# Kernel optimization log

Measured on AMD Instinct MI355X. Metric: run time of the kernel, lower is better.

## Reference

```python
import jax, jax.numpy as jnp
import numpy as np


def conv2d_nchw(x, w, b, padding):
    # x: [B,Cin,H,W], w: [Cout,Cin,kh,kw]
    y = jax.lax.conv_general_dilated(
        x, w, window_strides=(1, 1), padding=padding,
        dimension_numbers=("NCHW", "OIHW", "NCHW"))
    return y + b[None, :, None, None]


def setup_inputs() -> dict:
    key = jax.random.key(0)
    ks = jax.random.split(key, 8)
    B, C, H, W = 8, 512, 50, 76
    A = 9  # 3 scales x 3 ratios
    base_feat = jax.random.normal(ks[0], (B, C, H, W), dtype=jnp.float32)
    im_info = jnp.tile(jnp.array([800.0, 1216.0, 1.0], jnp.float32), (B, 1))
    gt_boxes = jax.random.uniform(ks[1], (B, 20, 5), dtype=jnp.float32) * 100.0
    num_boxes = jax.random.randint(ks[2], (B,), 1, 20, dtype=jnp.int32)
    # learned parameters (Kaiming-ish small init)
    conv_w = jax.random.normal(ks[3], (512, C, 3, 3), dtype=jnp.float32) * 0.01
    conv_b = jnp.zeros((512,), jnp.float32)
    cls_w = jax.random.normal(ks[4], (2 * A, 512, 1, 1), dtype=jnp.float32) * 0.01
    cls_b = jnp.zeros((2 * A,), jnp.float32)
    bbox_w = jax.random.normal(ks[5], (4 * A, 512, 1, 1), dtype=jnp.float32) * 0.01
    bbox_b = jnp.zeros((4 * A,), jnp.float32)
    return dict(base_feat=base_feat, im_info=im_info, gt_boxes=gt_boxes,
                num_boxes=num_boxes, conv_w=conv_w, conv_b=conv_b,
                cls_w=cls_w, cls_b=cls_b, bbox_w=bbox_w, bbox_b=bbox_b)


def reference(base_feat, im_info, gt_boxes, num_boxes,
              conv_w, conv_b, cls_w, cls_b, bbox_w, bbox_b):
    # RPN_Conv 3x3 + ReLU
    rpn_conv = jax.nn.relu(conv2d_nchw(base_feat, conv_w, conv_b, "SAME"))
    # 1x1 cls head -> [B, 2A, H, W]
    rpn_cls_score = conv2d_nchw(rpn_conv, cls_w, cls_b, "VALID")
    B, C2, H, W = rpn_cls_score.shape
    # _RPN.reshape(x, 2): view as [B, 2, A*H, W], softmax over the 2-way dim
    score_rs = rpn_cls_score.reshape(B, 2, (C2 // 2) * H, W)
    prob_rs = jax.nn.softmax(score_rs, axis=1)
    rpn_cls_prob = prob_rs.reshape(B, C2, H, W)
    # 1x1 bbox head -> [B, 4A, H, W]
    rpn_bbox_pred = conv2d_nchw(rpn_conv, bbox_w, bbox_b, "VALID")
    return rpn_cls_prob, rpn_bbox_pred
```

## Files before the change

### kernel.cpp

```cpp
#include <hip/hip_runtime.h>
#include <hip/hip_bf16.h>


typedef __bf16 bf16_t;
typedef __attribute__((ext_vector_type(8))) __bf16 bf16x8;
typedef __attribute__((ext_vector_type(4))) __bf16 bf16x4;
typedef __attribute__((ext_vector_type(4))) float f32x4;

#define HW 3800
#define NPOS (8 * HW)
#define XP_IMG (52 * 78 * 512)

__device__ __forceinline__ void gload_lds16(const bf16_t* g, char* l) {
  __builtin_amdgcn_global_load_lds(
      (const __attribute__((address_space(1))) unsigned int*)g,
      (__attribute__((address_space(3))) unsigned int*)l, 16, 0, 0);
}

__global__ __launch_bounds__(256) void pad_nhwc(const float* __restrict__ x,
                                                bf16_t* __restrict__ Xp) {
  const int t = threadIdx.x;
  const int blk = blockIdx.x;
  if (blk < 1600) {
    __shared__ __align__(16) bf16_t tile[76][136];
    const int cb = blk & 3;
    int r = blk >> 2;
    const int h = r % 50, b = r / 50;
#pragma unroll
    for (int it = 0; it < 10; ++it) {
      int idx = it * 256 + t;
      if (idx < 2432) {
        int c = idx / 19, w4 = idx - c * 19;
        const float4 v = *(const float4*)(x +
            (((size_t)(b * 512 + cb * 128 + c)) * 50 + h) * 76 + w4 * 4);
        tile[w4 * 4 + 0][c] = (bf16_t)v.x;
        tile[w4 * 4 + 1][c] = (bf16_t)v.y;
        tile[w4 * 4 + 2][c] = (bf16_t)v.z;
        tile[w4 * 4 + 3][c] = (bf16_t)v.w;
      }
    }
    __syncthreads();
#pragma unroll
    for (int it = 0; it < 5; ++it) {
      int idx = it * 256 + t;
      if (idx < 1216) {
        int w = idx >> 4, c8 = idx & 15;
        bf16x8 v = *(const bf16x8*)&tile[w][c8 * 8];
        *(bf16x8*)(Xp + ((size_t)(b * 52 + h + 1) * 78 + (w + 1)) * 512 +
                   cb * 128 + c8 * 8) = v;
      }
    }
  } else {
    const int blk2 = blk - 1600;
    const int b = blk2 >> 1, half = blk2 & 1;
    bf16x8 z;
#pragma unroll
    for (int j = 0; j < 8; ++j) z[j] = (bf16_t)0.f;
#pragma unroll
    for (int it = 0; it < 32; ++it) {
      int idx = it * 256 + t;
      int q = half * 128 + (idx >> 6);
      int c8 = idx & 63;
      int h, w;
      if (q < 78)       { h = 0;           w = q; }
      else if (q < 156) { h = 51;          w = q - 78; }
      else if (q < 206) { h = q - 156 + 1; w = 0; }
      else              { h = q - 206 + 1; w = 77; }
      *(bf16x8*)(Xp + ((size_t)(b * 52 + h) * 78 + w) * 512 + c8 * 8) = z;
    }
  }
}

__global__ __launch_bounds__(256) void wtrans(const float* __restrict__ cw,
                                              bf16_t* __restrict__ Wt) {
  __shared__ bf16_t lw[4608];
  const int t = threadIdx.x;
  const int co = blockIdx.x;
  const float* src = cw + (size_t)co * 4608;
#pragma unroll
  for (int it = 0; it < 18; ++it) {
    int idx = it * 256 + t;
    lw[idx] = (bf16_t)src[idx];
  }
  __syncthreads();
#pragma unroll
  for (int s = 0; s < 9; ++s) {
    int ci = t * 2;
    bf16_t v0 = lw[ci * 9 + s], v1 = lw[(ci + 1) * 9 + s];
    bf16_t* dst = Wt + ((size_t)s * 512 + co) * 512 + ci;
    dst[0] = v0; dst[1] = v1;
  }
}

__global__ __launch_bounds__(256) void whb_build(const float* __restrict__ clsw,
                                                 const float* __restrict__ boxw,
                                                 bf16_t* __restrict__ Whb) {
  int t = blockIdx.x * 256 + threadIdx.x;
  int ci = t & 511; int row = t >> 9;
  float v = 0.f;
  if (row < 18) {
    int a = row >> 1, logit = row & 1;
    v = clsw[(logit * 9 + a) * 512 + ci];
  } else if (row < 54) {
    v = boxw[(row - 18) * 512 + ci];
  }
  Whb[(size_t)row * 512 + ci] = (bf16_t)v;
}

__global__ __launch_bounds__(512) void conv3x3(const bf16_t* __restrict__ Xp,
                                               const bf16_t* __restrict__ Wt,
                                               const float* __restrict__ convb,
                                               bf16_t* __restrict__ rc2) {
  __shared__ __align__(16) char smem[131072];
  const int tid = threadIdx.x;
  const int lane = tid & 63;
  const int wv = tid >> 6;
  const int wm = wv >> 2;
  const int wn = wv & 3;
  const int lm = lane & 15, lg = lane >> 4;

  const int raw = blockIdx.x;
  const int wg = (raw & 7) * 30 + (raw >> 3);
  const int b = wg / 30;
  const int rem = wg - b * 30;
  const int co_base = (rem & 1) * 256;
  const int pos_base = (rem >> 1) * 256;

  int aSrc[4], hB[4], wB[4], cB[4];
#pragma unroll
  for (int i = 0; i < 4; ++i) {
    int d = i * 512 + tid;
    int r = d >> 3, p = d & 7, c = p ^ (r & 7);
    aSrc[i] = (co_base + r) * 512 + c * 8;
    int m = pos_base + r; if (m > HW - 1) m = HW - 1;
    hB[i] = m / 76; wB[i] = m - (m / 76) * 76; cB[i] = c * 8;
  }
  const bf16_t* XpB = Xp + (size_t)b * XP_IMG;

  int aOff[8], bOff[4], koffs[2];
#pragma unroll
  for (int m = 0; m < 8; ++m) aOff[m] = (wm * 128 + m * 16 + lm) * 128;
#pragma unroll
  for (int n = 0; n < 4; ++n) bOff[n] = 32768 + (wn * 64 + n * 16 + lm) * 128;
#pragma unroll
  for (int ks = 0; ks < 2; ++ks) koffs[ks] = ((ks * 4 + lg) ^ (lm & 7)) << 4;

  f32x4 acc[8][4];
#pragma unroll
  for (int i = 0; i < 8; ++i)
#pragma unroll
    for (int j = 0; j < 4; ++j) acc[i][j] = (f32x4){0.f, 0.f, 0.f, 0.f};

#pragma unroll
  for (int i = 0; i < 4; ++i)
    gload_lds16(Wt + aSrc[i], smem + (i * 512 + tid) * 16);
#pragma unroll
  for (int i = 0; i < 4; ++i)
    gload_lds16(XpB + (hB[i] * 78 + wB[i]) * 512 + cB[i],
                smem + 32768 + (i * 512 + tid) * 16);
  asm volatile("s_waitcnt vmcnt(0)" ::: "memory");
  __builtin_amdgcn_s_barrier();
  __builtin_amdgcn_sched_barrier(0);

  for (int kt = 0; kt < 72; ++kt) {
    const int cur = kt & 1;
    const char* Ab = smem + cur * 65536;
    char* Anxt = smem + (cur ^ 1) * 65536;
    const int tn = kt + 1;
    const int sn = tn >> 3, cbn = tn & 7;

    bf16x8 pa[4], pb[4];

    if (tn < 72) {
      const bf16_t* As = Wt + (size_t)sn * 262144 + cbn * 64;
#pragma unroll
      for (int i = 0; i < 4; ++i)
        gload_lds16(As + aSrc[i], Anxt + (i * 512 + tid) * 16);
    }
#pragma unroll
    for (int n = 0; n < 4; ++n) pb[n] = *(const bf16x8*)(Ab + bOff[n] + koffs[0]);
#pragma unroll
    for (int f = 0; f < 4; ++f) pa[f] = *(const bf16x8*)(Ab + aOff[f] + koffs[0]);
    __builtin_amdgcn_s_setprio(1);
#pragma unroll
    for (int f = 0; f < 4; ++f)
#pragma unroll
      for (int n = 0; n < 4; ++n)
        acc[f][n] = __builtin_amdgcn_mfma_f32_16x16x32_bf16(pa[f], pb[n], acc[f][n], 0, 0, 0);
    __builtin_amdgcn_s_setprio(0);
    __builtin_amdgcn_s_barrier();

    if (tn < 72) {
      const int kh = sn / 3, kw = sn - kh * 3;
#pragma unroll
      for (int i = 0; i < 4; ++i) {
        int off = ((hB[i] + kh) * 78 + (wB[i] + kw)) * 512 + cB[i] + cbn * 64;
        gload_lds16(XpB + off, Anxt + 32768 + (i * 512 + tid) * 16);
      }
    }
#pragma unroll
    for (int f = 0; f < 4; ++f) pa[f] = *(const bf16x8*)(Ab + aOff[4 + f] + koffs[0]);
    __builtin_amdgcn_s_setprio(1);
#pragma unroll
    for (int f = 0; f < 4; ++f)
#pragma unroll
      for (int n = 0; n < 4; ++n)
        acc[4 + f][n] = __builtin_amdgcn_mfma_f32_16x16x32_bf16(pa[f], pb[n], acc[4 + f][n], 0, 0, 0);
    __builtin_amdgcn_s_setprio(0);
    __builtin_amdgcn_s_barrier();

#pragma unroll
    for (int n = 0; n < 4; ++n) pb[n] = *(const bf16x8*)(Ab + bOff[n] + koffs[1]);
#pragma unroll
    for (int f = 0; f < 4; ++f) pa[f] = *(const bf16x8*)(Ab + aOff[f] + koffs[1]);
    __builtin_amdgcn_s_setprio(1);
#pragma unroll
    for (int f = 0; f < 4; ++f)
#pragma unroll
      for (int n = 0; n < 4; ++n)
        acc[f][n] = __builtin_amdgcn_mfma_f32_16x16x32_bf16(pa[f], pb[n], acc[f][n], 0, 0, 0);
    __builtin_amdgcn_s_setprio(0);
    __builtin_amdgcn_s_barrier();

#pragma unroll
    for (int f = 0; f < 4; ++f) pa[f] = *(const bf16x8*)(Ab + aOff[4 + f] + koffs[1]);
    __builtin_amdgcn_s_setprio(1);
#pragma unroll
    for (int f = 0; f < 4; ++f)
#pragma unroll
      for (int n = 0; n < 4; ++n)
        acc[4 + f][n] = __builtin_amdgcn_mfma_f32_16x16x32_bf16(pa[f], pb[n], acc[4 + f][n], 0, 0, 0);
    __builtin_amdgcn_s_setprio(0);

    asm volatile("s_waitcnt vmcnt(0)" ::: "memory");
    __builtin_amdgcn_s_barrier();
    __builtin_amdgcn_sched_barrier(0);
  }

  const size_t outRow = (size_t)b * HW;
#pragma unroll
  for (int m = 0; m < 8; ++m) {
    const int co = co_base + wm * 128 + m * 16 + lg * 4;
    const float4 bias = *(const float4*)(convb + co);
#pragma unroll
    for (int n = 0; n < 4; ++n) {
      const int pos = pos_base + wn * 64 + n * 16 + lm;
      if (pos < HW) {
        bf16x4 v;
        float z0 = acc[m][n][0] + bias.x; v[0] = (bf16_t)(z0 > 0.f ? z0 : 0.f);
        float z1 = acc[m][n][1] + bias.y; v[1] = (bf16_t)(z1 > 0.f ? z1 : 0.f);
        float z2 = acc[m][n][2] + bias.z; v[2] = (bf16_t)(z2 > 0.f ? z2 : 0.f);
        float z3 = acc[m][n][3] + bias.w; v[3] = (bf16_t)(z3 > 0.f ? z3 : 0.f);
        *(bf16x4*)(rc2 + (outRow + pos) * 512 + co) = v;
      }
    }
  }
}

__global__ __launch_bounds__(256) void heads_mfma(const bf16_t* __restrict__ rc2,
                                                  const bf16_t* __restrict__ Whb,
                                                  const float* __restrict__ clsb,
                                                  const float* __restrict__ boxb,
                                                  float* __restrict__ out) {
  __shared__ __align__(16) char smem[24576];
  const int t = threadIdx.x, lane = t & 63, wv = t >> 6;
  const int lm = lane & 15, lg = lane >> 4, lx = lane & 7;
  const int pos_base = blockIdx.x * 128;

  int aSrc[2], bSrc[4];
#pragma unroll
  for (int i = 0; i < 2; ++i) {
    int d = i * 256 + t;
    int r = d >> 3, p = d & 7, c = p ^ (r & 7);
    aSrc[i] = r * 512 + c * 8;
  }
#pragma unroll
  for (int i = 0; i < 4; ++i) {
    int d = i * 256 + t;
    int r = d >> 3, p = d & 7, c = p ^ (r & 7);
    int pg = pos_base + r; if (pg > NPOS - 1) pg = NPOS - 1;
    bSrc[i] = pg * 512 + c * 8;
  }

  f32x4 acc[4][2];
#pragma unroll
  for (int i = 0; i < 4; ++i)
#pragma unroll
    for (int j = 0; j < 2; ++j) acc[i][j] = (f32x4){0.f, 0.f, 0.f, 0.f};

  for (int cb = 0; cb < 8; ++cb) {
    __syncthreads();
#pragma unroll
    for (int i = 0; i < 2; ++i) {
      int d = i * 256 + t;
      gload_lds16(Whb + aSrc[i] + cb * 64, &smem[d * 16]);
    }
#pragma unroll
    for (int i = 0; i < 4; ++i) {
      int d = i * 256 + t;
      gload_lds16(rc2 + (size_t)bSrc[i] + cb * 64, &smem[8192 + d * 16]);
    }
    __syncthreads();
#pragma unroll
    for (int ks = 0; ks < 2; ++ks) {
      const int koff = ((ks * 4 + lg) ^ lx) << 4;
      bf16x8 af[4], bfr[2];
#pragma unroll
      for (int f = 0; f < 4; ++f)
        af[f] = *(const bf16x8*)&smem[(f * 16 + lm) * 128 + koff];
#pragma unroll
      for (int f = 0; f < 2; ++f)
        bfr[f] = *(const bf16x8*)&smem[8192 + (wv * 32 + f * 16 + lm) * 128 + koff];
#pragma unroll
      for (int fa = 0; fa < 4; ++fa)
#pragma unroll
        for (int fb = 0; fb < 2; ++fb)
          acc[fa][fb] = __builtin_amdgcn_mfma_f32_16x16x32_bf16(
              af[fa], bfr[fb], acc[fa][fb], 0, 0, 0);
    }
  }

  float* boxOut = out + (size_t)8 * 18 * HW;
#pragma unroll
  for (int fb = 0; fb < 2; ++fb) {
    const int pg = pos_base + wv * 32 + fb * 16 + lm;
    if (pg < NPOS) {
      const int b = pg / HW;
      const int m = pg - b * HW;
#pragma unroll
      for (int fa = 0; fa < 4; ++fa) {
        const int base = fa * 16 + lg * 4;
#pragma unroll
        for (int pr = 0; pr < 2; ++pr) {
          const int row0 = base + pr * 2;
          const float v0 = acc[fa][fb][pr * 2];
          const float v1 = acc[fa][fb][pr * 2 + 1];
          if (row0 < 18) {
            const int a = row0 >> 1;
            const float s0 = v0 + clsb[a];
            const float s1 = v1 + clsb[9 + a];
            const float mx = fmaxf(s0, s1);
            const float e0 = expf(s0 - mx), e1 = expf(s1 - mx);
            const float inv = 1.0f / (e0 + e1);
            out[((size_t)(b * 18 + a)) * HW + m] = e0 * inv;
            out[((size_t)(b * 18 + 9 + a)) * HW + m] = e1 * inv;
          } else if (row0 < 54) {
            const int c0 = row0 - 18;
            boxOut[((size_t)(b * 36 + c0)) * HW + m] = v0 + boxb[c0];
            boxOut[((size_t)(b * 36 + c0 + 1)) * HW + m] = v1 + boxb[c0 + 1];
          }
        }
      }
    }
  }
}

extern "C" void kernel_launch(void* const* d_in, const int* in_sizes, int n_in,
                              void* d_out, int out_size, void* d_ws, size_t ws_size,
                              hipStream_t stream) {
  (void)in_sizes; (void)n_in; (void)out_size; (void)ws_size;
  const float* base_feat = (const float*)d_in[0];
  const float* conv_w = (const float*)d_in[4];
  const float* conv_b = (const float*)d_in[5];
  const float* cls_w  = (const float*)d_in[6];
  const float* cls_b  = (const float*)d_in[7];
  const float* bbox_w = (const float*)d_in[8];
  const float* bbox_b = (const float*)d_in[9];

  char* ws = (char*)d_ws;
  bf16_t* Xp  = (bf16_t*)(ws);
  bf16_t* Wt  = (bf16_t*)(ws + 33226752);
  bf16_t* rc2 = (bf16_t*)(ws + 37945344);
  bf16_t* Whb = (bf16_t*)(ws + 69074944);

  hipLaunchKernelGGL(pad_nhwc,   dim3(1616), dim3(256), 0, stream, base_feat, Xp);
  hipLaunchKernelGGL(wtrans,     dim3(512),  dim3(256), 0, stream, conv_w, Wt);
  hipLaunchKernelGGL(whb_build,  dim3(128),  dim3(256), 0, stream, cls_w, bbox_w, Whb);
  hipLaunchKernelGGL(conv3x3,    dim3(240),  dim3(512), 0, stream, Xp, Wt, conv_b, rc2);
  hipLaunchKernelGGL(heads_mfma, dim3(238),  dim3(256), 0, stream, rc2, Whb, cls_b, bbox_b,
                     (float*)d_out);
}
```

Baseline: 162.1 us.

## Switch conv3x3 mainloop to triple-buffered K=32 stages with prefetch depth two

```diff
diff --git a/kernel.cpp b/kernel.cpp
--- a/kernel.cpp
+++ b/kernel.cpp
@@ -111,7 +111,7 @@
                                                const bf16_t* __restrict__ Wt,
                                                const float* __restrict__ convb,
                                                bf16_t* __restrict__ rc2) {
-  __shared__ __align__(16) char smem[131072];
+  __shared__ __align__(16) char smem[98304];
   const int tid = threadIdx.x;
   const int lane = tid & 63;
   const int wv = tid >> 6;
@@ -126,24 +126,23 @@
   const int co_base = (rem & 1) * 256;
   const int pos_base = (rem >> 1) * 256;
 
-  int aSrc[4], hB[4], wB[4], cB[4];
-#pragma unroll
-  for (int i = 0; i < 4; ++i) {
+  int aSrcRow[2], hB2[2], wB2[2], cB2[2];
+#pragma unroll
+  for (int i = 0; i < 2; ++i) {
     int d = i * 512 + tid;
-    int r = d >> 3, p = d & 7, c = p ^ (r & 7);
-    aSrc[i] = (co_base + r) * 512 + c * 8;
+    int r = d >> 2, p = d & 3, c = p ^ ((r >> 1) & 3);
+    aSrcRow[i] = (co_base + r) * 512 + c * 8;
     int m = pos_base + r; if (m > HW - 1) m = HW - 1;
-    hB[i] = m / 76; wB[i] = m - (m / 76) * 76; cB[i] = c * 8;
+    hB2[i] = m / 76; wB2[i] = m - (m / 76) * 76; cB2[i] = c * 8;
   }
   const bf16_t* XpB = Xp + (size_t)b * XP_IMG;
 
-  int aOff[8], bOff[4], koffs[2];
-#pragma unroll
-  for (int m = 0; m < 8; ++m) aOff[m] = (wm * 128 + m * 16 + lm) * 128;
-#pragma unroll
-  for (int n = 0; n < 4; ++n) bOff[n] = 32768 + (wn * 64 + n * 16 + lm) * 128;
-#pragma unroll
-  for (int ks = 0; ks < 2; ++ks) koffs[ks] = ((ks * 4 + lg) ^ (lm & 7)) << 4;
+  const int koff = (lg ^ ((lm >> 1) & 3)) << 4;
+  int aOffF[8], bOffF[4];
+#pragma unroll
+  for (int m = 0; m < 8; ++m) aOffF[m] = (wm * 128 + m * 16 + lm) * 64 + koff;
+#pragma unroll
+  for (int n = 0; n < 4; ++n) bOffF[n] = 16384 + (wn * 64 + n * 16 + lm) * 64 + koff;
 
   f32x4 acc[8][4];
 #pragma unroll
@@ -151,91 +150,71 @@
 #pragma unroll
     for (int j = 0; j < 4; ++j) acc[i][j] = (f32x4){0.f, 0.f, 0.f, 0.f};
 
-#pragma unroll
-  for (int i = 0; i < 4; ++i)
-    gload_lds16(Wt + aSrc[i], smem + (i * 512 + tid) * 16);
-#pragma unroll
-  for (int i = 0; i < 4; ++i)
-    gload_lds16(XpB + (hB[i] * 78 + wB[i]) * 512 + cB[i],
-                smem + 32768 + (i * 512 + tid) * 16);
-  asm volatile("s_waitcnt vmcnt(0)" ::: "memory");
+#define ISSUE_STAGE(KT, BASE) {                                                   \
+    const int s_ = (KT) >> 4, cb_ = (KT) & 15;                                    \
+    const int kh_ = s_ / 3, kw_ = s_ - kh_ * 3;                                   \
+    const bf16_t* As_ = Wt + (size_t)s_ * 262144 + cb_ * 32;                      \
+    _Pragma("unroll")                                                             \
+    for (int i = 0; i < 2; ++i)                                                   \
+      gload_lds16(As_ + aSrcRow[i], smem + (BASE) + (i * 512 + tid) * 16);        \
+    _Pragma("unroll")                                                             \
+    for (int i = 0; i < 2; ++i)                                                   \
+      gload_lds16(XpB + ((hB2[i] + kh_) * 78 + (wB2[i] + kw_)) * 512 + cB2[i] +   \
+                      cb_ * 32,                                                   \
+                  smem + (BASE) + 16384 + (i * 512 + tid) * 16);                  \
+  }
+
+#define TILE(KT, CURB, NXTB, DO_ISSUE, LAST) {                                    \
+    if (DO_ISSUE) ISSUE_STAGE((KT) + 2, NXTB);                                    \
+    const char* Ab_ = smem + (CURB);                                              \
+    bf16x8 pb_[4], pa_[4];                                                        \
+    _Pragma("unroll")                                                             \
+    for (int n = 0; n < 4; ++n) pb_[n] = *(const bf16x8*)(Ab_ + bOffF[n]);        \
+    _Pragma("unroll")                                                             \
+    for (int f = 0; f < 4; ++f) pa_[f] = *(const bf16x8*)(Ab_ + aOffF[f]);        \
+    __builtin_amdgcn_s_setprio(1);                                                \
+    _Pragma("unroll")                                                             \
+    for (int f = 0; f < 4; ++f)                                                   \
+      _Pragma("unroll")                                                           \
+      for (int n = 0; n < 4; ++n)                                                 \
+        acc[f][n] = __builtin_amdgcn_mfma_f32_16x16x32_bf16(pa_[f], pb_[n],       \
+                                                            acc[f][n], 0, 0, 0); \
+    __builtin_amdgcn_s_setprio(0);                                                \
+    _Pragma("unroll")                                                             \
+    for (int f = 0; f < 4; ++f) pa_[f] = *(const bf16x8*)(Ab_ + aOffF[4 + f]);    \
+    __builtin_amdgcn_s_setprio(1);                                                \
+    _Pragma("unroll")                                                             \
+    for (int f = 0; f < 4; ++f)                                                   \
+      _Pragma("unroll")                                                           \
+      for (int n = 0; n < 4; ++n)                                                 \
+        acc[4 + f][n] = __builtin_amdgcn_mfma_f32_16x16x32_bf16(pa_[f], pb_[n],   \
+                                                          acc[4 + f][n], 0, 0, 0);\
+    __builtin_amdgcn_s_setprio(0);                                                \
+    if (!(LAST)) {                                                                \
+      if (DO_ISSUE) { asm volatile("s_waitcnt vmcnt(4)" ::: "memory"); }          \
+      else          { asm volatile("s_waitcnt vmcnt(0)" ::: "memory"); }          \
+      __builtin_amdgcn_s_barrier();                                               \
+      __builtin_amdgcn_sched_barrier(0);                                          \
+    }                                                                             \
+  }
+
+  ISSUE_STAGE(0, 0);
+  ISSUE_STAGE(1, 32768);
+  asm volatile("s_waitcnt vmcnt(4)" ::: "memory");
   __builtin_amdgcn_s_barrier();
   __builtin_amdgcn_sched_barrier(0);
 
-  for (int kt = 0; kt < 72; ++kt) {
-    const int cur = kt & 1;
-    const char* Ab = smem + cur * 65536;
-    char* Anxt = smem + (cur ^ 1) * 65536;
-    const int tn = kt + 1;
-    const int sn = tn >> 3, cbn = tn & 7;
-
-    bf16x8 pa[4], pb[4];
-
-    if (tn < 72) {
-      const bf16_t* As = Wt + (size_t)sn * 262144 + cbn * 64;
-#pragma unroll
-      for (int i = 0; i < 4; ++i)
-        gload_lds16(As + aSrc[i], Anxt + (i * 512 + tid) * 16);
-    }
-#pragma unroll
-    for (int n = 0; n < 4; ++n) pb[n] = *(const bf16x8*)(Ab + bOff[n] + koffs[0]);
-#pragma unroll
-    for (int f = 0; f < 4; ++f) pa[f] = *(const bf16x8*)(Ab + aOff[f] + koffs[0]);
-    __builtin_amdgcn_s_setprio(1);
-#pragma unroll
-    for (int f = 0; f < 4; ++f)
-#pragma unroll
-      for (int n = 0; n < 4; ++n)
-        acc[f][n] = __builtin_amdgcn_mfma_f32_16x16x32_bf16(pa[f], pb[n], acc[f][n], 0, 0, 0);
-    __builtin_amdgcn_s_setprio(0);
-    __builtin_amdgcn_s_barrier();
-
-    if (tn < 72) {
-      const int kh = sn / 3, kw = sn - kh * 3;
-#pragma unroll
-      for (int i = 0; i < 4; ++i) {
-        int off = ((hB[i] + kh) * 78 + (wB[i] + kw)) * 512 + cB[i] + cbn * 64;
-        gload_lds16(XpB + off, Anxt + 32768 + (i * 512 + tid) * 16);
-      }
-    }
-#pragma unroll
-    for (int f = 0; f < 4; ++f) pa[f] = *(const bf16x8*)(Ab + aOff[4 + f] + koffs[0]);
-    __builtin_amdgcn_s_setprio(1);
-#pragma unroll
-    for (int f = 0; f < 4; ++f)
-#pragma unroll
-      for (int n = 0; n < 4; ++n)
-        acc[4 + f][n] = __builtin_amdgcn_mfma_f32_16x16x32_bf16(pa[f], pb[n], acc[4 + f][n], 0, 0, 0);
-    __builtin_amdgcn_s_setprio(0);
-    __builtin_amdgcn_s_barrier();
-
-#pragma unroll
-    for (int n = 0; n < 4; ++n) pb[n] = *(const bf16x8*)(Ab + bOff[n] + koffs[1]);
-#pragma unroll
-    for (int f = 0; f < 4; ++f) pa[f] = *(const bf16x8*)(Ab + aOff[f] + koffs[1]);
-    __builtin_amdgcn_s_setprio(1);
-#pragma unroll
-    for (int f = 0; f < 4; ++f)
-#pragma unroll
-      for (int n = 0; n < 4; ++n)
-        acc[f][n] = __builtin_amdgcn_mfma_f32_16x16x32_bf16(pa[f], pb[n], acc[f][n], 0, 0, 0);
-    __builtin_amdgcn_s_setprio(0);
-    __builtin_amdgcn_s_barrier();
-
-#pragma unroll
-    for (int f = 0; f < 4; ++f) pa[f] = *(const bf16x8*)(Ab + aOff[4 + f] + koffs[1]);
-    __builtin_amdgcn_s_setprio(1);
-#pragma unroll
-    for (int f = 0; f < 4; ++f)
-#pragma unroll
-      for (int n = 0; n < 4; ++n)
-        acc[4 + f][n] = __builtin_amdgcn_mfma_f32_16x16x32_bf16(pa[f], pb[n], acc[4 + f][n], 0, 0, 0);
-    __builtin_amdgcn_s_setprio(0);
-
-    asm volatile("s_waitcnt vmcnt(0)" ::: "memory");
-    __builtin_amdgcn_s_barrier();
-    __builtin_amdgcn_sched_barrier(0);
-  }
+  for (int kt = 0; kt < 141; kt += 3) {
+    TILE(kt + 0, 0,     65536, true, false);
+    TILE(kt + 1, 32768, 0,     true, false);
+    TILE(kt + 2, 65536, 32768, true, false);
+  }
+  TILE(141, 0,     65536, true,  false);
+  TILE(142, 32768, 0,     false, false);
+  TILE(143, 65536, 32768, false, true);
+
+#undef TILE
+#undef ISSUE_STAGE
 
   const size_t outRow = (size_t)b * HW;
 #pragma unroll
```

New measurement: 164.2 us. About the same (+1.3%).

## Prefetch two K-tiles ahead in conv3x3 with in-place staged LDS reloads

Applied to the files above, without the earlier changes.

```diff
diff --git a/kernel.cpp b/kernel.cpp
--- a/kernel.cpp
+++ b/kernel.cpp
@@ -107,10 +107,10 @@
   Whb[(size_t)row * 512 + ci] = (bf16_t)v;
 }
 
-__global__ __launch_bounds__(512) void conv3x3(const bf16_t* __restrict__ Xp,
-                                               const bf16_t* __restrict__ Wt,
-                                               const float* __restrict__ convb,
-                                               bf16_t* __restrict__ rc2) {
+__global__ __launch_bounds__(512, 2) void conv3x3(const bf16_t* __restrict__ Xp,
+                                                  const bf16_t* __restrict__ Wt,
+                                                  const float* __restrict__ convb,
+                                                  bf16_t* __restrict__ rc2) {
   __shared__ __align__(16) char smem[131072];
   const int tid = threadIdx.x;
   const int lane = tid & 63;
@@ -125,25 +125,38 @@
   const int rem = wg - b * 30;
   const int co_base = (rem & 1) * 256;
   const int pos_base = (rem >> 1) * 256;
-
-  int aSrc[4], hB[4], wB[4], cB[4];
+  const bf16_t* XpB = Xp + (size_t)b * XP_IMG;
+
+  int aSrc[4];
 #pragma unroll
   for (int i = 0; i < 4; ++i) {
     int d = i * 512 + tid;
-    int r = d >> 3, p = d & 7, c = p ^ (r & 7);
+    int r = d >> 3, c = (d & 7) ^ (r & 7);
     aSrc[i] = (co_base + r) * 512 + c * 8;
-    int m = pos_base + r; if (m > HW - 1) m = HW - 1;
-    hB[i] = m / 76; wB[i] = m - (m / 76) * 76; cB[i] = c * 8;
-  }
-  const bf16_t* XpB = Xp + (size_t)b * XP_IMG;
-
-  int aOff[8], bOff[4], koffs[2];
+  }
+  int bSpa[2][2], bCc[2][2], bDst[2][2];
+#pragma unroll
+  for (int f = 0; f < 2; ++f)
+#pragma unroll
+    for (int i = 0; i < 2; ++i) {
+      int d = i * 512 + tid;
+      int rl = d >> 3;
+      int rp = ((rl >> 5) << 6) + f * 32 + (rl & 31);
+      int c = (d & 7) ^ (rp & 7);
+      int m = pos_base + rp; if (m > HW - 1) m = HW - 1;
+      int h = m / 76, w = m - (m / 76) * 76;
+      bSpa[f][i] = h * 78 + w;
+      bCc[f][i] = c * 8;
+      bDst[f][i] = rp * 128 + (d & 7) * 16;
+    }
+
+  const int koff0 = (lg ^ (lm & 7)) << 4;
+  const int koff1 = ((4 + lg) ^ (lm & 7)) << 4;
+  int aOff[8], bOff[4];
 #pragma unroll
   for (int m = 0; m < 8; ++m) aOff[m] = (wm * 128 + m * 16 + lm) * 128;
 #pragma unroll
   for (int n = 0; n < 4; ++n) bOff[n] = 32768 + (wn * 64 + n * 16 + lm) * 128;
-#pragma unroll
-  for (int ks = 0; ks < 2; ++ks) koffs[ks] = ((ks * 4 + lg) ^ (lm & 7)) << 4;
 
   f32x4 acc[8][4];
 #pragma unroll
@@ -151,91 +164,116 @@
 #pragma unroll
     for (int j = 0; j < 4; ++j) acc[i][j] = (f32x4){0.f, 0.f, 0.f, 0.f};
 
-#pragma unroll
-  for (int i = 0; i < 4; ++i)
-    gload_lds16(Wt + aSrc[i], smem + (i * 512 + tid) * 16);
-#pragma unroll
-  for (int i = 0; i < 4; ++i)
-    gload_lds16(XpB + (hB[i] * 78 + wB[i]) * 512 + cB[i],
-                smem + 32768 + (i * 512 + tid) * 16);
-  asm volatile("s_waitcnt vmcnt(0)" ::: "memory");
+#define STAGE_A(KT, BASE) {                                                     \
+    const int s_ = (KT) >> 3, cb_ = (KT) & 7;                                   \
+    const bf16_t* As_ = Wt + (size_t)s_ * 262144 + cb_ * 64;                    \
+    _Pragma("unroll")                                                           \
+    for (int i_ = 0; i_ < 4; ++i_)                                              \
+      gload_lds16(As_ + aSrc[i_], (BASE) + (i_ * 512 + tid) * 16);              \
+  }
+#define STAGE_B(KT, BASE, F) {                                                  \
+    const int s_ = (KT) >> 3, cb_ = (KT) & 7;                                   \
+    const int sp_ = (s_ / 3) * 78 + (s_ - (s_ / 3) * 3);                        \
+    _Pragma("unroll")                                                           \
+    for (int i_ = 0; i_ < 2; ++i_)                                              \
+      gload_lds16(XpB + (size_t)(bSpa[F][i_] + sp_) * 512 + bCc[F][i_] +        \
+                      cb_ * 64,                                                 \
+                  (BASE) + 32768 + bDst[F][i_]);                                \
+  }
+
+  STAGE_A(0, smem);        STAGE_B(0, smem, 0);        STAGE_B(0, smem, 1);
+  STAGE_A(1, smem + 65536); STAGE_B(1, smem + 65536, 0); STAGE_B(1, smem + 65536, 1);
+  asm volatile("s_waitcnt vmcnt(8)" ::: "memory");
   __builtin_amdgcn_s_barrier();
   __builtin_amdgcn_sched_barrier(0);
 
-  for (int kt = 0; kt < 72; ++kt) {
-    const int cur = kt & 1;
-    const char* Ab = smem + cur * 65536;
-    char* Anxt = smem + (cur ^ 1) * 65536;
-    const int tn = kt + 1;
-    const int sn = tn >> 3, cbn = tn & 7;
-
-    bf16x8 pa[4], pb[4];
-
-    if (tn < 72) {
-      const bf16_t* As = Wt + (size_t)sn * 262144 + cbn * 64;
-#pragma unroll
-      for (int i = 0; i < 4; ++i)
-        gload_lds16(As + aSrc[i], Anxt + (i * 512 + tid) * 16);
-    }
-#pragma unroll
-    for (int n = 0; n < 4; ++n) pb[n] = *(const bf16x8*)(Ab + bOff[n] + koffs[0]);
-#pragma unroll
-    for (int f = 0; f < 4; ++f) pa[f] = *(const bf16x8*)(Ab + aOff[f] + koffs[0]);
+  bf16x8 ar[4][2], br[4][2];
+  for (int t = 0; t < 72; ++t) {
+    char* base = smem + (t & 1) * 65536;
+    const int tn = t + 2;
+    const bool st = (tn < 72);
+
+#pragma unroll
+    for (int n = 0; n < 2; ++n) {
+      br[n][0] = *(const bf16x8*)(base + bOff[n] + koff0);
+      br[n][1] = *(const bf16x8*)(base + bOff[n] + koff1);
+    }
+#pragma unroll
+    for (int m = 0; m < 4; ++m) {
+      ar[m][0] = *(const bf16x8*)(base + aOff[m] + koff0);
+      ar[m][1] = *(const bf16x8*)(base + aOff[m] + koff1);
+    }
     __builtin_amdgcn_s_setprio(1);
 #pragma unroll
-    for (int f = 0; f < 4; ++f)
-#pragma unroll
-      for (int n = 0; n < 4; ++n)
-        acc[f][n] = __builtin_amdgcn_mfma_f32_16x16x32_bf16(pa[f], pb[n], acc[f][n], 0, 0, 0);
+    for (int m = 0; m < 4; ++m)
+#pragma unroll
+      for (int n = 0; n < 2; ++n)
+#pragma unroll
+        for (int ks = 0; ks < 2; ++ks)
+          acc[m][n] = __builtin_amdgcn_mfma_f32_16x16x32_bf16(
+              ar[m][ks], br[n][ks], acc[m][n], 0, 0, 0);
     __builtin_amdgcn_s_setprio(0);
     __builtin_amdgcn_s_barrier();
-
-    if (tn < 72) {
-      const int kh = sn / 3, kw = sn - kh * 3;
-#pragma unroll
-      for (int i = 0; i < 4; ++i) {
-        int off = ((hB[i] + kh) * 78 + (wB[i] + kw)) * 512 + cB[i] + cbn * 64;
-        gload_lds16(XpB + off, Anxt + 32768 + (i * 512 + tid) * 16);
-      }
-    }
-#pragma unroll
-    for (int f = 0; f < 4; ++f) pa[f] = *(const bf16x8*)(Ab + aOff[4 + f] + koffs[0]);
+    __builtin_amdgcn_sched_barrier(0);
+
+    if (st) STAGE_B(tn, base, 0);
+#pragma unroll
+    for (int n = 2; n < 4; ++n) {
+      br[n][0] = *(const bf16x8*)(base + bOff[n] + koff0);
+      br[n][1] = *(const bf16x8*)(base + bOff[n] + koff1);
+    }
     __builtin_amdgcn_s_setprio(1);
 #pragma unroll
-    for (int f = 0; f < 4; ++f)
-#pragma unroll
-      for (int n = 0; n < 4; ++n)
-        acc[4 + f][n] = __builtin_amdgcn_mfma_f32_16x16x32_bf16(pa[f], pb[n], acc[4 + f][n], 0, 0, 0);
+    for (int m = 0; m < 4; ++m)
+#pragma unroll
+      for (int n = 2; n < 4; ++n)
+#pragma unroll
+        for (int ks = 0; ks < 2; ++ks)
+          acc[m][n] = __builtin_amdgcn_mfma_f32_16x16x32_bf16(
+              ar[m][ks], br[n][ks], acc[m][n], 0, 0, 0);
     __builtin_amdgcn_s_setprio(0);
     __builtin_amdgcn_s_barrier();
-
-#pragma unroll
-    for (int n = 0; n < 4; ++n) pb[n] = *(const bf16x8*)(Ab + bOff[n] + koffs[1]);
-#pragma unroll
-    for (int f = 0; f < 4; ++f) pa[f] = *(const bf16x8*)(Ab + aOff[f] + koffs[1]);
+    __builtin_amdgcn_sched_barrier(0);
+
+    if (st) STAGE_B(tn, base, 1);
+#pragma unroll
+    for (int m = 0; m < 4; ++m) {
+      ar[m][0] = *(const bf16x8*)(base + aOff[4 + m] + koff0);
+      ar[m][1] = *(const bf16x8*)(base + aOff[4 + m] + koff1);
+    }
     __builtin_amdgcn_s_setprio(1);
 #pragma unroll
-    for (int f = 0; f < 4; ++f)
-#pragma unroll
-      for (int n = 0; n < 4; ++n)
-        acc[f][n] = __builtin_amdgcn_mfma_f32_16x16x32_bf16(pa[f], pb[n], acc[f][n], 0, 0, 0);
+    for (int m = 0; m < 4; ++m)
+#pragma unroll
+      for (int n = 2; n < 4; ++n)
+#pragma unroll
+        for (int ks = 0; ks < 2; ++ks)
+          acc[4 + m][n] = __builtin_amdgcn_mfma_f32_16x16x32_bf16(
+              ar[m][ks], br[n][ks], acc[4 + m][n], 0, 0, 0);
     __builtin_amdgcn_s_setprio(0);
     __builtin_amdgcn_s_barrier();
-
-#pragma unroll
-    for (int f = 0; f < 4; ++f) pa[f] = *(const bf16x8*)(Ab + aOff[4 + f] + koffs[1]);
+    __builtin_amdgcn_sched_barrier(0);
+
+    if (st) STAGE_A(tn, base);
     __builtin_amdgcn_s_setprio(1);
 #pragma unroll
-    for (int f = 0; f < 4; ++f)
-#pragma unroll
-      for (int n = 0; n < 4; ++n)
-        acc[4 + f][n] = __builtin_amdgcn_mfma_f32_16x16x32_bf16(pa[f], pb[n], acc[4 + f][n], 0, 0, 0);
+    for (int m = 0; m < 4; ++m)
+#pragma unroll
+      for (int n = 0; n < 2; ++n)
+#pragma unroll
+        for (int ks = 0; ks < 2; ++ks)
+          acc[4 + m][n] = __builtin_amdgcn_mfma_f32_16x16x32_bf16(
+              ar[m][ks], br[n][ks], acc[4 + m][n], 0, 0, 0);
     __builtin_amdgcn_s_setprio(0);
 
-    asm volatile("s_waitcnt vmcnt(0)" ::: "memory");
+    if (t == 71) break;
+    if (t < 70) { asm volatile("s_waitcnt vmcnt(8)" ::: "memory"); }
+    else        { asm volatile("s_waitcnt vmcnt(0)" ::: "memory"); }
     __builtin_amdgcn_s_barrier();
     __builtin_amdgcn_sched_barrier(0);
   }
+#undef STAGE_A
+#undef STAGE_B
 
   const size_t outRow = (size_t)b * HW;
 #pragma unroll
```

New measurement: 165.9 us. 1.02x slower.

## Stream conv weights directly into registers and halve LDS staging

Applied to the files above, without the earlier changes.

```diff
diff --git a/kernel.cpp b/kernel.cpp
--- a/kernel.cpp
+++ b/kernel.cpp
@@ -107,11 +107,11 @@
   Whb[(size_t)row * 512 + ci] = (bf16_t)v;
 }
 
-__global__ __launch_bounds__(512) void conv3x3(const bf16_t* __restrict__ Xp,
-                                               const bf16_t* __restrict__ Wt,
-                                               const float* __restrict__ convb,
-                                               bf16_t* __restrict__ rc2) {
-  __shared__ __align__(16) char smem[131072];
+__global__ __launch_bounds__(512, 2) void conv3x3(const bf16_t* __restrict__ Xp,
+                                                  const bf16_t* __restrict__ Wt,
+                                                  const float* __restrict__ convb,
+                                                  bf16_t* __restrict__ rc2) {
+  __shared__ __align__(16) char smem[65536];
   const int tid = threadIdx.x;
   const int lane = tid & 63;
   const int wv = tid >> 6;
@@ -125,25 +125,25 @@
   const int rem = wg - b * 30;
   const int co_base = (rem & 1) * 256;
   const int pos_base = (rem >> 1) * 256;
-
-  int aSrc[4], hB[4], wB[4], cB[4];
+  const bf16_t* XpB = Xp + (size_t)b * XP_IMG;
+
+  int hB[4], wB[4], cB[4];
 #pragma unroll
   for (int i = 0; i < 4; ++i) {
     int d = i * 512 + tid;
-    int r = d >> 3, p = d & 7, c = p ^ (r & 7);
-    aSrc[i] = (co_base + r) * 512 + c * 8;
+    int r = d >> 3, c = (d & 7) ^ (r & 7);
     int m = pos_base + r; if (m > HW - 1) m = HW - 1;
     hB[i] = m / 76; wB[i] = m - (m / 76) * 76; cB[i] = c * 8;
   }
-  const bf16_t* XpB = Xp + (size_t)b * XP_IMG;
-
-  int aOff[8], bOff[4], koffs[2];
-#pragma unroll
-  for (int m = 0; m < 8; ++m) aOff[m] = (wm * 128 + m * 16 + lm) * 128;
-#pragma unroll
-  for (int n = 0; n < 4; ++n) bOff[n] = 32768 + (wn * 64 + n * 16 + lm) * 128;
-#pragma unroll
-  for (int ks = 0; ks < 2; ++ks) koffs[ks] = ((ks * 4 + lg) ^ (lm & 7)) << 4;
+
+  int bOff[4][2];
+#pragma unroll
+  for (int n = 0; n < 4; ++n)
+#pragma unroll
+    for (int ks = 0; ks < 2; ++ks)
+      bOff[n][ks] = (wn * 64 + n * 16 + lm) * 128 + (((ks * 4 + lg) ^ (lm & 7)) << 4);
+
+  const bf16_t* aBase = Wt + (size_t)(co_base + wm * 128 + lm) * 512 + lg * 8;
 
   f32x4 acc[8][4];
 #pragma unroll
@@ -151,91 +151,80 @@
 #pragma unroll
     for (int j = 0; j < 4; ++j) acc[i][j] = (f32x4){0.f, 0.f, 0.f, 0.f};
 
-#pragma unroll
-  for (int i = 0; i < 4; ++i)
-    gload_lds16(Wt + aSrc[i], smem + (i * 512 + tid) * 16);
-#pragma unroll
-  for (int i = 0; i < 4; ++i)
-    gload_lds16(XpB + (hB[i] * 78 + wB[i]) * 512 + cB[i],
-                smem + 32768 + (i * 512 + tid) * 16);
-  asm volatile("s_waitcnt vmcnt(0)" ::: "memory");
+#define STAGE_B(KT, BASE) {                                                     \
+    const int s_ = (KT) >> 3, cb_ = (KT) & 7;                                   \
+    const int kh_ = s_ / 3, kw_ = s_ - kh_ * 3;                                 \
+    _Pragma("unroll")                                                           \
+    for (int i_ = 0; i_ < 4; ++i_)                                              \
+      gload_lds16(XpB + (size_t)((hB[i_] + kh_) * 78 + (wB[i_] + kw_)) * 512 +  \
+                      cB[i_] + cb_ * 64,                                        \
+                  (BASE) + (i_ * 512 + tid) * 16);                              \
+  }
+#define LOAD_A(KT, DST, HF) {                                                   \
+    const int s_ = (KT) >> 3, cb_ = (KT) & 7;                                   \
+    const bf16_t* p_ = aBase + (size_t)s_ * 262144 + (size_t)(HF) * 64 * 512 +  \
+                       cb_ * 64;                                                \
+    _Pragma("unroll")                                                           \
+    for (int m_ = 0; m_ < 4; ++m_)                                              \
+      _Pragma("unroll")                                                         \
+      for (int ks_ = 0; ks_ < 2; ++ks_)                                         \
+        DST[m_ * 2 + ks_] = *(const bf16x8*)(p_ + m_ * 16 * 512 + ks_ * 32);    \
+  }
+
+  bf16x8 a0[8], a1[8], bfr[4][2];
+
+  STAGE_B(0, smem);
+  LOAD_A(0, a0, 0);
+  LOAD_A(0, a1, 1);
+  asm volatile("s_waitcnt vmcnt(16)" ::: "memory");
   __builtin_amdgcn_s_barrier();
   __builtin_amdgcn_sched_barrier(0);
 
-  for (int kt = 0; kt < 72; ++kt) {
-    const int cur = kt & 1;
-    const char* Ab = smem + cur * 65536;
-    char* Anxt = smem + (cur ^ 1) * 65536;
-    const int tn = kt + 1;
-    const int sn = tn >> 3, cbn = tn & 7;
-
-    bf16x8 pa[4], pb[4];
-
-    if (tn < 72) {
-      const bf16_t* As = Wt + (size_t)sn * 262144 + cbn * 64;
-#pragma unroll
-      for (int i = 0; i < 4; ++i)
-        gload_lds16(As + aSrc[i], Anxt + (i * 512 + tid) * 16);
-    }
-#pragma unroll
-    for (int n = 0; n < 4; ++n) pb[n] = *(const bf16x8*)(Ab + bOff[n] + koffs[0]);
-#pragma unroll
-    for (int f = 0; f < 4; ++f) pa[f] = *(const bf16x8*)(Ab + aOff[f] + koffs[0]);
+  for (int t = 0; t < 72; ++t) {
+    const char* base = smem + (t & 1) * 32768;
+    char* nxt = smem + ((t + 1) & 1) * 32768;
+    const bool more = (t < 71);
+
+    if (more) STAGE_B(t + 1, nxt);
+
+#pragma unroll
+    for (int n = 0; n < 4; ++n)
+#pragma unroll
+      for (int ks = 0; ks < 2; ++ks)
+        bfr[n][ks] = *(const bf16x8*)(base + bOff[n][ks]);
+
     __builtin_amdgcn_s_setprio(1);
 #pragma unroll
-    for (int f = 0; f < 4; ++f)
+    for (int m = 0; m < 4; ++m)
 #pragma unroll
       for (int n = 0; n < 4; ++n)
-        acc[f][n] = __builtin_amdgcn_mfma_f32_16x16x32_bf16(pa[f], pb[n], acc[f][n], 0, 0, 0);
+#pragma unroll
+        for (int ks = 0; ks < 2; ++ks)
+          acc[m][n] = __builtin_amdgcn_mfma_f32_16x16x32_bf16(
+              a0[m * 2 + ks], bfr[n][ks], acc[m][n], 0, 0, 0);
     __builtin_amdgcn_s_setprio(0);
-    __builtin_amdgcn_s_barrier();
-
-    if (tn < 72) {
-      const int kh = sn / 3, kw = sn - kh * 3;
-#pragma unroll
-      for (int i = 0; i < 4; ++i) {
-        int off = ((hB[i] + kh) * 78 + (wB[i] + kw)) * 512 + cB[i] + cbn * 64;
-        gload_lds16(XpB + off, Anxt + 32768 + (i * 512 + tid) * 16);
-      }
-    }
-#pragma unroll
-    for (int f = 0; f < 4; ++f) pa[f] = *(const bf16x8*)(Ab + aOff[4 + f] + koffs[0]);
+    if (more) LOAD_A(t + 1, a0, 0);
+
     __builtin_amdgcn_s_setprio(1);
 #pragma unroll
-    for (int f = 0; f < 4; ++f)
+    for (int m = 0; m < 4; ++m)
 #pragma unroll
       for (int n = 0; n < 4; ++n)
-        acc[4 + f][n] = __builtin_amdgcn_mfma_f32_16x16x32_bf16(pa[f], pb[n], acc[4 + f][n], 0, 0, 0);
+#pragma unroll
+        for (int ks = 0; ks < 2; ++ks)
+          acc[4 + m][n] = __builtin_amdgcn_mfma_f32_16x16x32_bf16(
+              a1[m * 2 + ks], bfr[n][ks], acc[4 + m][n], 0, 0, 0);
     __builtin_amdgcn_s_setprio(0);
-    __builtin_amdgcn_s_barrier();
-
-#pragma unroll
-    for (int n = 0; n < 4; ++n) pb[n] = *(const bf16x8*)(Ab + bOff[n] + koffs[1]);
-#pragma unroll
-    for (int f = 0; f < 4; ++f) pa[f] = *(const bf16x8*)(Ab + aOff[f] + koffs[1]);
-    __builtin_amdgcn_s_setprio(1);
-#pragma unroll
-    for (int f = 0; f < 4; ++f)
-#pragma unroll
-      for (int n = 0; n < 4; ++n)
-        acc[f][n] = __builtin_amdgcn_mfma_f32_16x16x32_bf16(pa[f], pb[n], acc[f][n], 0, 0, 0);
-    __builtin_amdgcn_s_setprio(0);
-    __builtin_amdgcn_s_barrier();
-
-#pragma unroll
-    for (int f = 0; f < 4; ++f) pa[f] = *(const bf16x8*)(Ab + aOff[4 + f] + koffs[1]);
-    __builtin_amdgcn_s_setprio(1);
-#pragma unroll
-    for (int f = 0; f < 4; ++f)
-#pragma unroll
-      for (int n = 0; n < 4; ++n)
-        acc[4 + f][n] = __builtin_amdgcn_mfma_f32_16x16x32_bf16(pa[f], pb[n], acc[4 + f][n], 0, 0, 0);
-    __builtin_amdgcn_s_setprio(0);
-
-    asm volatile("s_waitcnt vmcnt(0)" ::: "memory");
+    if (more) LOAD_A(t + 1, a1, 1);
+
+    if (t == 71) break;
+    __builtin_amdgcn_sched_barrier(0);
+    asm volatile("s_waitcnt vmcnt(16)" ::: "memory");
     __builtin_amdgcn_s_barrier();
     __builtin_amdgcn_sched_barrier(0);
   }
+#undef STAGE_B
+#undef LOAD_A
 
   const size_t outRow = (size_t)b * HW;
 #pragma unroll
```

Result: slower. 340.8 us (+110.2%).
